# Kernel tuning notes

Measured on AMD Instinct MI355X. Metric: run time of the kernel, lower is better.

Reference implementation:

```python
import jax, jax.numpy as jnp
import numpy as np

D_MODEL = 2048
NUM_HEADS = 16
D_K = D_MODEL // NUM_HEADS
THETA = 10000.0
MAX_SEQ_LEN = 2048
GPT_INIT_STD = 0.02


def setup_inputs() -> dict:
    key = jax.random.key(0)
    ks = jax.random.split(key, 5)
    B, T = 4, 2048
    x = jax.random.normal(ks[0], (B, T, D_MODEL), dtype=jnp.float32)
    token_positions = jnp.arange(T, dtype=jnp.int64 if jax.config.jax_enable_x64 else jnp.int32)[None, :]
    Wq = jax.random.normal(ks[1], (D_MODEL, D_MODEL), dtype=jnp.float32) * GPT_INIT_STD
    Wk = jax.random.normal(ks[2], (D_MODEL, D_MODEL), dtype=jnp.float32) * GPT_INIT_STD
    Wv = jax.random.normal(ks[3], (D_MODEL, D_MODEL), dtype=jnp.float32) * GPT_INIT_STD
    Wo = jax.random.normal(ks[4], (D_MODEL, D_MODEL), dtype=jnp.float32) * GPT_INIT_STD
    return {"x": x, "token_positions": token_positions, "Wq": Wq, "Wk": Wk, "Wv": Wv, "Wo": Wo}


def _rope_tables(dtype):
    # angles[p, j] = p * theta^(-2j/d_k), j in [0, d_k/2)
    j = jnp.arange(D_K // 2, dtype=jnp.float32)
    inv_freq = THETA ** (-2.0 * j / float(D_K))
    pos = jnp.arange(MAX_SEQ_LEN, dtype=jnp.float32)[:, None]
    angles = pos * inv_freq[None, :]
    return jnp.cos(angles).astype(dtype), jnp.sin(angles).astype(dtype)


def _apply_rope(t, cos_pos, sin_pos):
    # t: (b, h, s, d); cos/sin: (1, s, d/2) -> broadcast over (b, h)
    even = t[..., 0::2]
    odd = t[..., 1::2]
    c = cos_pos[:, None, :, :]  # (1,1,s,d/2)
    s = sin_pos[:, None, :, :]
    rot_even = even * c - odd * s
    rot_odd = even * s + odd * c
    out = jnp.stack([rot_even, rot_odd], axis=-1)  # (b,h,s,d/2,2)
    return out.reshape(t.shape)


def reference(x, token_positions, Wq, Wk, Wv, Wo):
    B, T, D = x.shape
    H, d = NUM_HEADS, D_K
    q = (x @ Wq.T).reshape(B, T, H, d).transpose(0, 2, 1, 3)  # (b,h,t,d)
    k = (x @ Wk.T).reshape(B, T, H, d).transpose(0, 2, 1, 3)
    v = (x @ Wv.T).reshape(B, T, H, d).transpose(0, 2, 1, 3)

    cos_tab, sin_tab = _rope_tables(x.dtype)
    cos_pos = cos_tab[token_positions]  # (1, t, d/2)
    sin_pos = sin_tab[token_positions]
    q = _apply_rope(q, cos_pos, sin_pos)
    k = _apply_rope(k, cos_pos, sin_pos)

    # token_positions is strictly increasing and attention_mask is None,
    # so build_attention_mask returns None -> unmasked eager attention.
    scale = float(d) ** -0.5
    scores = jnp.einsum('bhtd,bhsd->bhts', q, k) * scale
    attn = jax.nn.softmax(scores.astype(jnp.float32), axis=-1).astype(q.dtype)
    out = jnp.einsum('bhts,bhsd->bhtd', attn, v)  # (b,h,t,d)
    out = out.transpose(0, 2, 1, 3).reshape(B, T, D)  # (b,t,h*d)
    return out @ Wo.T
```

## Files before the change

kernel.cpp:

```cpp
#include <hip/hip_runtime.h>
#include <hip/hip_bf16.h>
#include <hip/hip_fp16.h>
#include <math.h>

#define TSEQ   2048
#define DMODEL 2048
#define NHEAD  16
#define DHEAD  128
#define NBATCH 4
#define MROWS  (NBATCH*TSEQ)

typedef __attribute__((ext_vector_type(8))) short v8s;
typedef __attribute__((ext_vector_type(4))) float v4f;
typedef __attribute__((ext_vector_type(16))) float v16f;

#if __has_builtin(__builtin_amdgcn_exp2f)
#define EXP2(x) __builtin_amdgcn_exp2f(x)
#else
#define EXP2(x) __expf((x) * 0.6931471805599453f)
#endif

__device__ __forceinline__ unsigned short f2b(float f) {
  __hip_bfloat16 h = __float2bfloat16(f);
  return *reinterpret_cast<unsigned short*>(&h);
}
__device__ __forceinline__ float b2f(unsigned int u) {
  unsigned short us = (unsigned short)u;
  __hip_bfloat16 h = *reinterpret_cast<__hip_bfloat16*>(&us);
  return __bfloat162float(h);
}
__device__ __forceinline__ unsigned int cvtpk(float lo, float hi) {
  unsigned int r;
  asm("v_cvt_pk_bf16_f32 %0, %1, %2" : "=v"(r) : "v"(lo), "v"(hi));
  return r;
}
__device__ __forceinline__ void gload_lds16(const unsigned short* g, unsigned short* l) {
  __builtin_amdgcn_global_load_lds(
      (const __attribute__((address_space(1))) unsigned int*)g,
      (__attribute__((address_space(3))) unsigned int*)l, 16, 0, 0);
}

__global__ void prep_kernel(const float* __restrict__ x,  const float* __restrict__ Wq,
                            const float* __restrict__ Wk, const float* __restrict__ Wv,
                            const float* __restrict__ Wo, const int* __restrict__ pos,
                            unsigned short* __restrict__ xb,  unsigned short* __restrict__ wqb,
                            unsigned short* __restrict__ wkb, unsigned short* __restrict__ wvb,
                            unsigned short* __restrict__ wob,
                            unsigned int* __restrict__ ropeT) {
  const int blk = blockIdx.x, tid = threadIdx.x;
  if (blk < 32768) {
    const float* in; unsigned short* out; int lb;
    if      (blk < 16384) { in = x;  out = xb;  lb = blk; }
    else if (blk < 20480) { in = Wq; out = wqb; lb = blk - 16384; }
    else if (blk < 24576) { in = Wk; out = wkb; lb = blk - 20480; }
    else if (blk < 28672) { in = Wv; out = wvb; lb = blk - 24576; }
    else                  { in = Wo; out = wob; lb = blk - 28672; }
    int i = lb * 256 + tid;
    float4 v = reinterpret_cast<const float4*>(in)[i];
    ushort4 o;
    o.x = f2b(v.x); o.y = f2b(v.y); o.z = f2b(v.z); o.w = f2b(v.w);
    reinterpret_cast<ushort4*>(out)[i] = o;
  } else {
    int idx = (blk - 32768) * 256 + tid;
    int t = idx >> 6, j = idx & 63;
    float p = (float)pos[t];
    float inv_freq = expf((-2.0f * (float)j / 128.0f) * logf(10000.0f));
    float ang = p * inv_freq;
    __half2 h2 = __floats2half2_rn(cosf(ang), sinf(ang));
    ropeT[idx] = *reinterpret_cast<unsigned int*>(&h2);
  }
}

template<int MODE>
__global__ __launch_bounds__(512, 2) void gemm8(const unsigned short* __restrict__ A,
                                                const unsigned short* __restrict__ Bt,
                                                void* __restrict__ Cout,
                                                const unsigned int* __restrict__ ropeT) {
  __shared__ unsigned short SL[65536];
  const int tid = threadIdx.x;
  const int lane = tid & 63, wv = tid >> 6;
  const int wr = wv >> 2, wc = wv & 3;
  const int g = lane >> 4, r16 = lane & 15;
  const int r7 = r16 & 7;
  const int sl0 = (g ^ r7) << 3;
  const int sl1 = ((4 + g) ^ r7) << 3;

  const int nx = gridDim.x;
  const int nwg = nx * gridDim.y;
  const int lid = blockIdx.y * nx + blockIdx.x;
  const int q8 = nwg >> 3, r8 = nwg & 7;
  const int xcd = lid & 7, off = lid >> 3;
  const int nlid = (xcd < r8 ? xcd * (q8 + 1) : r8 * (q8 + 1) + (xcd - r8) * q8) + off;
  const int mrow0 = (nlid / nx) * 256;
  const int ncol0 = (nlid % nx) * 256;

  const int srow = tid >> 3;
  const int sslot = tid & 7;

  auto stA = [&](int kt, int b, int hf) {
    const int k0 = kt * 64;
#pragma unroll
    for (int j = 0; j < 2; ++j) {
      int r = hf * 128 + j * 64 + srow;
      int slot = sslot ^ (r & 7);
      gload_lds16(&A[(size_t)(mrow0 + r) * DMODEL + k0 + slot * 8],
                  &SL[b * 16384 + (hf * 128 + j * 64) * 64 + tid * 8]);
    }
  };
  auto stB = [&](int kt, int b, int hf) {
    const int k0 = kt * 64;
#pragma unroll
    for (int j = 0; j < 2; ++j) {
      int r = hf * 128 + j * 64 + srow;
      int slot = sslot ^ (r & 7);
      gload_lds16(&Bt[(size_t)(ncol0 + r) * DMODEL + k0 + slot * 8],
                  &SL[32768 + b * 16384 + (hf * 128 + j * 64) * 64 + tid * 8]);
    }
  };

  v4f zero = {0.f, 0.f, 0.f, 0.f};
  v4f acc[8][4];
#pragma unroll
  for (int m = 0; m < 8; ++m)
#pragma unroll
    for (int n = 0; n < 4; ++n) acc[m][n] = zero;

  stA(0, 0, 0); stA(0, 0, 1); stB(0, 0, 0); stB(0, 0, 1);
  stA(1, 1, 0); stA(1, 1, 1); stB(1, 1, 0); stB(1, 1, 1);
  asm volatile("s_waitcnt vmcnt(8)" ::: "memory");
  __builtin_amdgcn_s_barrier();

  v8s af[4][2], bf[4][2];
  const int arow = wr * 128 + r16;
  const int brow = wc * 64 + r16;

  for (int kt = 0; kt < DMODEL / 64; ++kt) {
    const int p = kt & 1;
    unsigned short* LA = SL + p * 16384;
    unsigned short* LB = SL + 32768 + p * 16384;

#pragma unroll
    for (int m = 0; m < 4; ++m) {
      af[m][0] = *(const v8s*)&LA[(arow + m * 16) * 64 + sl0];
      af[m][1] = *(const v8s*)&LA[(arow + m * 16) * 64 + sl1];
    }
#pragma unroll
    for (int n = 0; n < 2; ++n) {
      bf[n][0] = *(const v8s*)&LB[(brow + n * 16) * 64 + sl0];
      bf[n][1] = *(const v8s*)&LB[(brow + n * 16) * 64 + sl1];
    }
    __builtin_amdgcn_s_barrier();
    asm volatile("s_waitcnt lgkmcnt(0)" ::: "memory");
    __builtin_amdgcn_sched_barrier(0);
    __builtin_amdgcn_s_setprio(1);
#pragma unroll
    for (int m = 0; m < 4; ++m)
#pragma unroll
      for (int n = 0; n < 2; ++n) {
        acc[m][n] = __builtin_amdgcn_mfma_f32_16x16x32_bf16(af[m][0], bf[n][0], acc[m][n], 0, 0, 0);
        acc[m][n] = __builtin_amdgcn_mfma_f32_16x16x32_bf16(af[m][1], bf[n][1], acc[m][n], 0, 0, 0);
      }
    __builtin_amdgcn_s_setprio(0);
    __builtin_amdgcn_s_barrier();

#pragma unroll
    for (int n = 2; n < 4; ++n) {
      bf[n][0] = *(const v8s*)&LB[(brow + n * 16) * 64 + sl0];
      bf[n][1] = *(const v8s*)&LB[(brow + n * 16) * 64 + sl1];
    }
    __builtin_amdgcn_s_barrier();
    asm volatile("s_waitcnt lgkmcnt(0)" ::: "memory");
    __builtin_amdgcn_sched_barrier(0);
    __builtin_amdgcn_s_setprio(1);
#pragma unroll
    for (int m = 0; m < 4; ++m)
#pragma unroll
      for (int n = 2; n < 4; ++n) {
        acc[m][n] = __builtin_amdgcn_mfma_f32_16x16x32_bf16(af[m][0], bf[n][0], acc[m][n], 0, 0, 0);
        acc[m][n] = __builtin_amdgcn_mfma_f32_16x16x32_bf16(af[m][1], bf[n][1], acc[m][n], 0, 0, 0);
      }
    __builtin_amdgcn_s_setprio(0);
    __builtin_amdgcn_s_barrier();

#pragma unroll
    for (int m = 0; m < 4; ++m) {
      af[m][0] = *(const v8s*)&LA[(arow + 64 + m * 16) * 64 + sl0];
      af[m][1] = *(const v8s*)&LA[(arow + 64 + m * 16) * 64 + sl1];
    }
    if (kt < DMODEL / 64 - 2) { stB(kt + 2, p, 0); stB(kt + 2, p, 1); }
    __builtin_amdgcn_s_barrier();
    asm volatile("s_waitcnt lgkmcnt(0)" ::: "memory");
    __builtin_amdgcn_sched_barrier(0);
    __builtin_amdgcn_s_setprio(1);
#pragma unroll
    for (int m = 0; m < 4; ++m)
#pragma unroll
      for (int n = 2; n < 4; ++n) {
        acc[m + 4][n] = __builtin_amdgcn_mfma_f32_16x16x32_bf16(af[m][0], bf[n][0], acc[m + 4][n], 0, 0, 0);
        acc[m + 4][n] = __builtin_amdgcn_mfma_f32_16x16x32_bf16(af[m][1], bf[n][1], acc[m + 4][n], 0, 0, 0);
      }
    __builtin_amdgcn_s_setprio(0);
    __builtin_amdgcn_s_barrier();

    if (kt < DMODEL / 64 - 2) {
      stA(kt + 2, p, 0); stA(kt + 2, p, 1);
      asm volatile("s_waitcnt vmcnt(8)" ::: "memory");
    } else {
      asm volatile("s_waitcnt vmcnt(0)" ::: "memory");
    }
    __builtin_amdgcn_s_barrier();
    __builtin_amdgcn_s_setprio(1);
#pragma unroll
    for (int m = 0; m < 4; ++m)
#pragma unroll
      for (int n = 0; n < 2; ++n) {
        acc[m + 4][n] = __builtin_amdgcn_mfma_f32_16x16x32_bf16(af[m][0], bf[n][0], acc[m + 4][n], 0, 0, 0);
        acc[m + 4][n] = __builtin_amdgcn_mfma_f32_16x16x32_bf16(af[m][1], bf[n][1], acc[m + 4][n], 0, 0, 0);
      }
    __builtin_amdgcn_s_setprio(0);
    __builtin_amdgcn_s_barrier();
  }

  if (MODE <= 1) {
    unsigned short* reg = SL + wv * 4608;
    const int band = ncol0 + wc * 64;
    const int h2 = band >> 7;
    const int dd0 = band & 127;
    const int lr2b = lane >> 2, c4 = lane & 3;
    const float SC = 0.12751726f;
#pragma unroll
    for (int hf = 0; hf < 2; ++hf) {
#pragma unroll
      for (int m = 0; m < 4; ++m)
#pragma unroll
        for (int n = 0; n < 4; ++n)
#pragma unroll
          for (int r = 0; r < 4; ++r)
            reg[(m * 16 + g * 4 + r) * 72 + n * 16 + r16] = f2b(acc[hf * 4 + m][n][r]);
      asm volatile("s_waitcnt lgkmcnt(0)" ::: "memory");
      __builtin_amdgcn_sched_barrier(0);
#pragma unroll
      for (int ps = 0; ps < 4; ++ps) {
        int lr2 = ps * 16 + lr2b;
        v8s d0 = *(const v8s*)&reg[lr2 * 72 + c4 * 16];
        v8s d1 = *(const v8s*)&reg[lr2 * 72 + c4 * 16 + 8];
        int row = mrow0 + wr * 128 + hf * 64 + lr2;
        int t = row & (TSEQ - 1), bb = row >> 11;
        const uint4* tp = (const uint4*)&ropeT[(t << 6) + (dd0 >> 1) + c4 * 8];
        uint4 t0 = tp[0], t1 = tp[1];
        unsigned int ow[8];
#pragma unroll
        for (int k = 0; k < 8; ++k) {
          unsigned int cs = (k < 4) ? (&t0.x)[k] : (&t1.x)[k - 4];
          __half2 hcs = *reinterpret_cast<__half2*>(&cs);
          float c = __half2float(__low2half(hcs));
          float s = __half2float(__high2half(hcs));
          int kk = (k & 3) * 2;
          float e = (k < 4) ? b2f((unsigned short)d0[kk])     : b2f((unsigned short)d1[kk]);
          float o = (k < 4) ? b2f((unsigned short)d0[kk + 1]) : b2f((unsigned short)d1[kk + 1]);
          float re = e * c - o * s;
          float ro = e * s + o * c;
          if (MODE == 0) { re *= SC; ro *= SC; }
          ow[k] = cvtpk(re, ro);
        }
        unsigned short* dst = (unsigned short*)Cout +
            (((size_t)bb * NHEAD + h2) * TSEQ + t) * DHEAD + dd0 + c4 * 16;
        *(uint4*)dst = make_uint4(ow[0], ow[1], ow[2], ow[3]);
        *(uint4*)(dst + 8) = make_uint4(ow[4], ow[5], ow[6], ow[7]);
      }
      if (hf == 0) {
        asm volatile("s_waitcnt lgkmcnt(0)" ::: "memory");
        __builtin_amdgcn_sched_barrier(0);
      }
    }
  } else {
#pragma unroll
    for (int m = 0; m < 8; ++m) {
#pragma unroll
      for (int n = 0; n < 4; ++n) {
#pragma unroll
        for (int r = 0; r < 4; ++r) {
          int row = mrow0 + wr * 128 + m * 16 + g * 4 + r;
          int col = ncol0 + wc * 64 + n * 16 + r16;
          float val = acc[m][n][r];
          if (MODE == 2) {
            int hh = row >> 7, dd = row & (DHEAD - 1);
            int bb = col >> 11, tt = col & (TSEQ - 1);
            ((unsigned short*)Cout)[(((size_t)bb * NHEAD + hh) * DHEAD + dd) * TSEQ + tt] = f2b(val);
          } else {
            ((float*)Cout)[(size_t)row * DMODEL + col] = val;
          }
        }
      }
    }
  }
}

__global__ __launch_bounds__(256, 2) void attn_kernel(const unsigned short* __restrict__ Q,
                                                      const unsigned short* __restrict__ K,
                                                      const unsigned short* __restrict__ Vt,
                                                      unsigned short* __restrict__ O) {
  __shared__ unsigned short Ks[2][64 * 128];
  __shared__ unsigned short Vs[2][64 * 128];
  const int tid = threadIdx.x, lane = tid & 63, w = tid >> 6;
  const int hi = lane >> 5, l31 = lane & 31;
  const int bh = blockIdx.y;
  const int b = bh >> 4, h = bh & 15;
  const int qbase = blockIdx.x * 256;
  const size_t hb = (size_t)bh * TSEQ * DHEAD;
  const size_t vb = (size_t)bh * DHEAD * TSEQ;

  v8s qf0[8], qf1[8];
  {
    const int qr0 = qbase + w * 64 + l31;
#pragma unroll
    for (int dk = 0; dk < 8; ++dk) {
      qf0[dk] = *(const v8s*)&Q[hb + (size_t)qr0 * DHEAD + dk * 16 + hi * 8];
      qf1[dk] = *(const v8s*)&Q[hb + (size_t)(qr0 + 32) * DHEAD + dk * 16 + hi * 8];
    }
  }

  v16f Z16 = {0,0,0,0,0,0,0,0,0,0,0,0,0,0,0,0};
  v16f o0[4], o1[4];
#pragma unroll
  for (int d = 0; d < 4; ++d) { o0[d] = Z16; o1[d] = Z16; }
  float l0 = 0.0f, l1 = 0.0f;

  const unsigned short* ksrc;
  const unsigned short* vsrc;
  {
    int kr = tid >> 4, kc = (tid & 15) ^ (kr & 15);
    ksrc = K + hb + (size_t)kr * DHEAD + kc * 8;
    int lr = tid >> 4, sp = (tid & 15) ^ (lr & 15);
    int vr = 2 * lr + (sp >> 3), vg = sp & 7;
    vsrc = Vt + vb + (size_t)vr * TSEQ + vg * 8;
  }
  auto stage = [&](const unsigned short* kp, const unsigned short* vp, int buf) {
#pragma unroll
    for (int j = 0; j < 4; ++j) {
      gload_lds16(kp + (size_t)j * 16 * DHEAD, &Ks[buf][(j * 256 + tid) * 8]);
      gload_lds16(vp + (size_t)j * 32 * TSEQ, &Vs[buf][(j * 256 + tid) * 8]);
    }
  };

  stage(ksrc, vsrc, 0);
  asm volatile("s_waitcnt vmcnt(0)" ::: "memory");
  __builtin_amdgcn_s_barrier();

  for (int t = 0; t < TSEQ / 64; ++t) {
    const int p = t & 1;
    if (t < TSEQ / 64 - 1)
      stage(ksrc + (size_t)(t + 1) * 64 * DHEAD, vsrc + (size_t)(t + 1) * 64, p ^ 1);

    float rs0 = 0.f, rs1 = 0.f;
#pragma unroll
    for (int kvt = 0; kvt < 2; ++kvt) {
      v16f s0 = Z16, s1 = Z16;
      __builtin_amdgcn_s_setprio(1);
#pragma unroll
      for (int dk = 0; dk < 8; ++dk) {
        int krow = kvt * 32 + l31;
        v8s a = *(const v8s*)&Ks[p][krow * 128 + ((dk * 16 + hi * 8) ^ ((krow & 15) << 3))];
        s0 = __builtin_amdgcn_mfma_f32_32x32x16_bf16(a, qf0[dk], s0, 0, 0, 0);
        s1 = __builtin_amdgcn_mfma_f32_32x32x16_bf16(a, qf1[dk], s1, 0, 0, 0);
      }
      __builtin_amdgcn_s_setprio(0);

#pragma unroll
      for (int r = 0; r < 16; ++r) {
        float p0 = EXP2(s0[r]); s0[r] = p0; rs0 += p0;
        float p1 = EXP2(s1[r]); s1[r] = p1; rs1 += p1;
      }

      union { unsigned int u[4]; v8s v; } pa0, pb0, pa1, pb1;
      {
        unsigned int wk[8];
#pragma unroll
        for (int i = 0; i < 8; ++i) wk[i] = cvtpk(s0[2 * i], s0[2 * i + 1]);
        asm("v_permlane32_swap_b32 %0, %1" : "+v"(wk[0]), "+v"(wk[2]));
        asm("v_permlane32_swap_b32 %0, %1" : "+v"(wk[1]), "+v"(wk[3]));
        asm("v_permlane32_swap_b32 %0, %1" : "+v"(wk[4]), "+v"(wk[6]));
        asm("v_permlane32_swap_b32 %0, %1" : "+v"(wk[5]), "+v"(wk[7]));
        pa0.u[0] = wk[0]; pa0.u[1] = wk[1]; pa0.u[2] = wk[2]; pa0.u[3] = wk[3];
        pb0.u[0] = wk[4]; pb0.u[1] = wk[5]; pb0.u[2] = wk[6]; pb0.u[3] = wk[7];
      }
      {
        unsigned int wk[8];
#pragma unroll
        for (int i = 0; i < 8; ++i) wk[i] = cvtpk(s1[2 * i], s1[2 * i + 1]);
        asm("v_permlane32_swap_b32 %0, %1" : "+v"(wk[0]), "+v"(wk[2]));
        asm("v_permlane32_swap_b32 %0, %1" : "+v"(wk[1]), "+v"(wk[3]));
        asm("v_permlane32_swap_b32 %0, %1" : "+v"(wk[4]), "+v"(wk[6]));
        asm("v_permlane32_swap_b32 %0, %1" : "+v"(wk[5]), "+v"(wk[7]));
        pa1.u[0] = wk[0]; pa1.u[1] = wk[1]; pa1.u[2] = wk[2]; pa1.u[3] = wk[3];
        pb1.u[0] = wk[4]; pb1.u[1] = wk[5]; pb1.u[2] = wk[6]; pb1.u[3] = wk[7];
      }

      __builtin_amdgcn_s_setprio(1);
      const int g0 = kvt * 4 + hi;
#pragma unroll
      for (int d = 0; d < 4; ++d) {
        int drow = d * 32 + l31;
        int lr = drow >> 1;
        int x = (drow & 1) << 3;
        int sw = lr & 15;
        v8s vf0 = *(const v8s*)&Vs[p][lr * 128 + (((x | g0) ^ sw) << 3)];
        v8s vf1 = *(const v8s*)&Vs[p][lr * 128 + (((x | (g0 + 2)) ^ sw) << 3)];
        o0[d] = __builtin_amdgcn_mfma_f32_32x32x16_bf16(pa0.v, vf0, o0[d], 0, 0, 0);
        o0[d] = __builtin_amdgcn_mfma_f32_32x32x16_bf16(pb0.v, vf1, o0[d], 0, 0, 0);
        o1[d] = __builtin_amdgcn_mfma_f32_32x32x16_bf16(pa1.v, vf0, o1[d], 0, 0, 0);
        o1[d] = __builtin_amdgcn_mfma_f32_32x32x16_bf16(pb1.v, vf1, o1[d], 0, 0, 0);
      }
      __builtin_amdgcn_s_setprio(0);
    }
    l0 += rs0; l1 += rs1;

    asm volatile("s_waitcnt vmcnt(0)" ::: "memory");
    __builtin_amdgcn_s_barrier();
  }

#pragma unroll
  for (int r = 0; r < 16; ++r) {
    int qi = (r & 3) + 8 * (r >> 2) + 4 * hi;
    float lq0 = __shfl(l0, qi) + __shfl(l0, qi + 32);
    float lq1 = __shfl(l1, qi) + __shfl(l1, qi + 32);
    float i0 = 1.0f / lq0, i1 = 1.0f / lq1;
    int t0 = qbase + w * 64 + qi;
#pragma unroll
    for (int d = 0; d < 4; ++d) {
      O[((size_t)(b * TSEQ + t0)) * DMODEL + h * DHEAD + d * 32 + l31] = f2b(o0[d][r] * i0);
      O[((size_t)(b * TSEQ + t0 + 32)) * DMODEL + h * DHEAD + d * 32 + l31] = f2b(o1[d][r] * i1);
    }
  }
}

extern "C" void kernel_launch(void* const* d_in, const int* in_sizes, int n_in,
                              void* d_out, int out_size, void* d_ws, size_t ws_size,
                              hipStream_t stream) {
  const float* x  = (const float*)d_in[0];
  const int*   pos = (const int*)d_in[1];
  const float* Wq = (const float*)d_in[2];
  const float* Wk = (const float*)d_in[3];
  const float* Wv = (const float*)d_in[4];
  const float* Wo = (const float*)d_in[5];
  float* out = (float*)d_out;
  char* ws = (char*)d_ws;

  const size_t WBYTES = (size_t)DMODEL * DMODEL * 2;
  const size_t XBYTES = (size_t)MROWS * DMODEL * 2;
  unsigned short* wqb = (unsigned short*)(ws);
  unsigned short* wkb = (unsigned short*)(ws + WBYTES);
  unsigned short* wvb = (unsigned short*)(ws + 2 * WBYTES);
  unsigned short* wob = (unsigned short*)(ws + 3 * WBYTES);
  unsigned short* xb  = (unsigned short*)(ws + 4 * WBYTES);
  unsigned short* Qb  = (unsigned short*)(ws + 4 * WBYTES + XBYTES);
  unsigned short* Kb  = (unsigned short*)(ws + 4 * WBYTES + 2 * XBYTES);
  unsigned short* Vtb = (unsigned short*)(ws + 4 * WBYTES + 3 * XBYTES);
  unsigned int* ropeT = (unsigned int*)(ws + 4 * WBYTES + 4 * XBYTES);
  if (ws_size < 4 * WBYTES + 4 * XBYTES + (size_t)TSEQ * 64 * sizeof(unsigned int)) return;

  prep_kernel<<<33280, 256, 0, stream>>>(x, Wq, Wk, Wv, Wo, pos,
                                         xb, wqb, wkb, wvb, wob, ropeT);

  dim3 gg(DMODEL / 256, MROWS / 256);
  gemm8<0><<<gg, 512, 0, stream>>>(xb, wqb, (void*)Qb, ropeT);
  gemm8<1><<<gg, 512, 0, stream>>>(xb, wkb, (void*)Kb, ropeT);
  gemm8<2><<<dim3(MROWS / 256, DMODEL / 256), 512, 0, stream>>>(wvb, xb, (void*)Vtb, ropeT);

  attn_kernel<<<dim3(TSEQ / 256, 64), 256, 0, stream>>>(Qb, Kb, Vtb, xb);

  gemm8<3><<<gg, 512, 0, stream>>>(xb, wob, (void*)out, ropeT);
}
```

Baseline: 470.1 us.

## Halve attention query tile per block to 128 rows, one 32-row tile per wave

Each wave in the attention kernel now handles 32 query rows instead of 64, so a block covers 128 query rows and the grid doubles along the sequence axis. This cuts per-wave registers (one Q fragment set and one output accumulator set) and raises block count and occupancy. In exchange, each K/V tile staged into LDS is reused by half as many queries, which doubles total K/V global traffic and LDS fill work. The QK and PV phases are regrouped per 64-key tile.

```diff
diff --git a/kernel.cpp b/kernel.cpp
--- a/kernel.cpp
+++ b/kernel.cpp
@@ -306,25 +306,23 @@
   const int hi = lane >> 5, l31 = lane & 31;
   const int bh = blockIdx.y;
   const int b = bh >> 4, h = bh & 15;
-  const int qbase = blockIdx.x * 256;
+  const int qbase = blockIdx.x * 128;
   const size_t hb = (size_t)bh * TSEQ * DHEAD;
   const size_t vb = (size_t)bh * DHEAD * TSEQ;
 
-  v8s qf0[8], qf1[8];
+  v8s qf[8];
   {
-    const int qr0 = qbase + w * 64 + l31;
-#pragma unroll
-    for (int dk = 0; dk < 8; ++dk) {
-      qf0[dk] = *(const v8s*)&Q[hb + (size_t)qr0 * DHEAD + dk * 16 + hi * 8];
-      qf1[dk] = *(const v8s*)&Q[hb + (size_t)(qr0 + 32) * DHEAD + dk * 16 + hi * 8];
-    }
+    const int qrow = qbase + w * 32 + l31;
+#pragma unroll
+    for (int dk = 0; dk < 8; ++dk)
+      qf[dk] = *(const v8s*)&Q[hb + (size_t)qrow * DHEAD + dk * 16 + hi * 8];
   }
 
   v16f Z16 = {0,0,0,0,0,0,0,0,0,0,0,0,0,0,0,0};
-  v16f o0[4], o1[4];
-#pragma unroll
-  for (int d = 0; d < 4; ++d) { o0[d] = Z16; o1[d] = Z16; }
-  float l0 = 0.0f, l1 = 0.0f;
+  v16f o_acc[4];
+#pragma unroll
+  for (int d = 0; d < 4; ++d) o_acc[d] = Z16;
+  float l_run = 0.0f;
 
   const unsigned short* ksrc;
   const unsigned short* vsrc;
@@ -352,51 +350,48 @@
     if (t < TSEQ / 64 - 1)
       stage(ksrc + (size_t)(t + 1) * 64 * DHEAD, vsrc + (size_t)(t + 1) * 64, p ^ 1);
 
-    float rs0 = 0.f, rs1 = 0.f;
+    v16f s[2]; s[0] = Z16; s[1] = Z16;
+    __builtin_amdgcn_s_setprio(1);
 #pragma unroll
     for (int kvt = 0; kvt < 2; ++kvt) {
-      v16f s0 = Z16, s1 = Z16;
-      __builtin_amdgcn_s_setprio(1);
 #pragma unroll
       for (int dk = 0; dk < 8; ++dk) {
         int krow = kvt * 32 + l31;
         v8s a = *(const v8s*)&Ks[p][krow * 128 + ((dk * 16 + hi * 8) ^ ((krow & 15) << 3))];
-        s0 = __builtin_amdgcn_mfma_f32_32x32x16_bf16(a, qf0[dk], s0, 0, 0, 0);
-        s1 = __builtin_amdgcn_mfma_f32_32x32x16_bf16(a, qf1[dk], s1, 0, 0, 0);
-      }
-      __builtin_amdgcn_s_setprio(0);
-
+        s[kvt] = __builtin_amdgcn_mfma_f32_32x32x16_bf16(a, qf[dk], s[kvt], 0, 0, 0);
+      }
+    }
+    __builtin_amdgcn_s_setprio(0);
+
+    float rowsum = 0.f;
+#pragma unroll
+    for (int kvt = 0; kvt < 2; ++kvt)
 #pragma unroll
       for (int r = 0; r < 16; ++r) {
-        float p0 = EXP2(s0[r]); s0[r] = p0; rs0 += p0;
-        float p1 = EXP2(s1[r]); s1[r] = p1; rs1 += p1;
-      }
-
-      union { unsigned int u[4]; v8s v; } pa0, pb0, pa1, pb1;
-      {
-        unsigned int wk[8];
-#pragma unroll
-        for (int i = 0; i < 8; ++i) wk[i] = cvtpk(s0[2 * i], s0[2 * i + 1]);
-        asm("v_permlane32_swap_b32 %0, %1" : "+v"(wk[0]), "+v"(wk[2]));
-        asm("v_permlane32_swap_b32 %0, %1" : "+v"(wk[1]), "+v"(wk[3]));
-        asm("v_permlane32_swap_b32 %0, %1" : "+v"(wk[4]), "+v"(wk[6]));
-        asm("v_permlane32_swap_b32 %0, %1" : "+v"(wk[5]), "+v"(wk[7]));
-        pa0.u[0] = wk[0]; pa0.u[1] = wk[1]; pa0.u[2] = wk[2]; pa0.u[3] = wk[3];
-        pb0.u[0] = wk[4]; pb0.u[1] = wk[5]; pb0.u[2] = wk[6]; pb0.u[3] = wk[7];
-      }
-      {
-        unsigned int wk[8];
-#pragma unroll
-        for (int i = 0; i < 8; ++i) wk[i] = cvtpk(s1[2 * i], s1[2 * i + 1]);
-        asm("v_permlane32_swap_b32 %0, %1" : "+v"(wk[0]), "+v"(wk[2]));
-        asm("v_permlane32_swap_b32 %0, %1" : "+v"(wk[1]), "+v"(wk[3]));
-        asm("v_permlane32_swap_b32 %0, %1" : "+v"(wk[4]), "+v"(wk[6]));
-        asm("v_permlane32_swap_b32 %0, %1" : "+v"(wk[5]), "+v"(wk[7]));
-        pa1.u[0] = wk[0]; pa1.u[1] = wk[1]; pa1.u[2] = wk[2]; pa1.u[3] = wk[3];
-        pb1.u[0] = wk[4]; pb1.u[1] = wk[5]; pb1.u[2] = wk[6]; pb1.u[3] = wk[7];
-      }
-
-      __builtin_amdgcn_s_setprio(1);
+        float pp = EXP2(s[kvt][r]);
+        s[kvt][r] = pp; rowsum += pp;
+      }
+    l_run += rowsum;
+
+    union { unsigned int u[4]; v8s v; } pf[4];
+#pragma unroll
+    for (int kvt = 0; kvt < 2; ++kvt) {
+      unsigned int wk[8];
+#pragma unroll
+      for (int i = 0; i < 8; ++i) wk[i] = cvtpk(s[kvt][2 * i], s[kvt][2 * i + 1]);
+      asm("v_permlane32_swap_b32 %0, %1" : "+v"(wk[0]), "+v"(wk[2]));
+      asm("v_permlane32_swap_b32 %0, %1" : "+v"(wk[1]), "+v"(wk[3]));
+      asm("v_permlane32_swap_b32 %0, %1" : "+v"(wk[4]), "+v"(wk[6]));
+      asm("v_permlane32_swap_b32 %0, %1" : "+v"(wk[5]), "+v"(wk[7]));
+      pf[2 * kvt].u[0] = wk[0]; pf[2 * kvt].u[1] = wk[1];
+      pf[2 * kvt].u[2] = wk[2]; pf[2 * kvt].u[3] = wk[3];
+      pf[2 * kvt + 1].u[0] = wk[4]; pf[2 * kvt + 1].u[1] = wk[5];
+      pf[2 * kvt + 1].u[2] = wk[6]; pf[2 * kvt + 1].u[3] = wk[7];
+    }
+
+    __builtin_amdgcn_s_setprio(1);
+#pragma unroll
+    for (int kvt = 0; kvt < 2; ++kvt) {
       const int g0 = kvt * 4 + hi;
 #pragma unroll
       for (int d = 0; d < 4; ++d) {
@@ -406,14 +401,11 @@
         int sw = lr & 15;
         v8s vf0 = *(const v8s*)&Vs[p][lr * 128 + (((x | g0) ^ sw) << 3)];
         v8s vf1 = *(const v8s*)&Vs[p][lr * 128 + (((x | (g0 + 2)) ^ sw) << 3)];
-        o0[d] = __builtin_amdgcn_mfma_f32_32x32x16_bf16(pa0.v, vf0, o0[d], 0, 0, 0);
-        o0[d] = __builtin_amdgcn_mfma_f32_32x32x16_bf16(pb0.v, vf1, o0[d], 0, 0, 0);
-        o1[d] = __builtin_amdgcn_mfma_f32_32x32x16_bf16(pa1.v, vf0, o1[d], 0, 0, 0);
-        o1[d] = __builtin_amdgcn_mfma_f32_32x32x16_bf16(pb1.v, vf1, o1[d], 0, 0, 0);
-      }
-      __builtin_amdgcn_s_setprio(0);
-    }
-    l0 += rs0; l1 += rs1;
+        o_acc[d] = __builtin_amdgcn_mfma_f32_32x32x16_bf16(pf[2 * kvt].v, vf0, o_acc[d], 0, 0, 0);
+        o_acc[d] = __builtin_amdgcn_mfma_f32_32x32x16_bf16(pf[2 * kvt + 1].v, vf1, o_acc[d], 0, 0, 0);
+      }
+    }
+    __builtin_amdgcn_s_setprio(0);
 
     asm volatile("s_waitcnt vmcnt(0)" ::: "memory");
     __builtin_amdgcn_s_barrier();
@@ -422,14 +414,12 @@
 #pragma unroll
   for (int r = 0; r < 16; ++r) {
     int qi = (r & 3) + 8 * (r >> 2) + 4 * hi;
-    float lq0 = __shfl(l0, qi) + __shfl(l0, qi + 32);
-    float lq1 = __shfl(l1, qi) + __shfl(l1, qi + 32);
-    float i0 = 1.0f / lq0, i1 = 1.0f / lq1;
-    int t0 = qbase + w * 64 + qi;
+    float lq = __shfl(l_run, qi) + __shfl(l_run, qi + 32);
+    float inv = 1.0f / lq;
+    int t = qbase + w * 32 + qi;
 #pragma unroll
     for (int d = 0; d < 4; ++d) {
-      O[((size_t)(b * TSEQ + t0)) * DMODEL + h * DHEAD + d * 32 + l31] = f2b(o0[d][r] * i0);
-      O[((size_t)(b * TSEQ + t0 + 32)) * DMODEL + h * DHEAD + d * 32 + l31] = f2b(o1[d][r] * i1);
+      O[((size_t)(b * TSEQ + t)) * DMODEL + h * DHEAD + d * 32 + l31] = f2b(o_acc[d][r] * inv);
     }
   }
 }
@@ -467,7 +457,7 @@
   gemm8<1><<<gg, 512, 0, stream>>>(xb, wkb, (void*)Kb, ropeT);
   gemm8<2><<<dim3(MROWS / 256, DMODEL / 256), 512, 0, stream>>>(wvb, xb, (void*)Vtb, ropeT);
 
-  attn_kernel<<<dim3(TSEQ / 256, 64), 256, 0, stream>>>(Qb, Kb, Vtb, xb);
+  attn_kernel<<<dim3(TSEQ / 128, 64), 256, 0, stream>>>(Qb, Kb, Vtb, xb);
 
   gemm8<3><<<gg, 512, 0, stream>>>(xb, wob, (void*)out, ropeT);
 }
```

After: 468.2 us (median of 2 runs). About the same (-0.4%).
